# Kernel tuning notes

Measured on AMD Instinct MI355X. Metric: run time of the kernel, lower is better.

The kernel has to match this reference:

```python
import jax, jax.numpy as jnp
import numpy as np

N = 100_000   # nodes
C = 32        # classes
E = 3_200_000 # edges


def setup_inputs() -> dict:
    key = jax.random.key(0)
    k1, k2, k3, k4, k5 = jax.random.split(key, 5)
    edge_index = jax.random.randint(k1, (2, E), 0, N, dtype=jnp.int32)
    edge_weight = jax.random.uniform(k2, (E,), dtype=jnp.float32) + 0.1  # positive weights
    inputs = jax.random.normal(k3, (N, C), dtype=jnp.float32)
    labels = jax.random.randint(k4, (N,), 0, C)
    y = jax.nn.one_hot(labels, C, dtype=jnp.float32)  # torch.where(y[:, i]) implies one-hot labels
    sample_mask = jax.random.bernoulli(k5, 0.5, (N,))
    return {"edge_index": edge_index, "edge_weight": edge_weight,
            "inputs": inputs, "y": y, "sample_mask": sample_mask}


def _normalize_sparse(edge_index, edge_weight, n):
    # normalize_sparse_tensor: add self-loops (weight 1), then D^{-1/2} A D^{-1/2}
    loop = jnp.arange(n, dtype=edge_index.dtype)
    row = jnp.concatenate([edge_index[0], loop])
    col = jnp.concatenate([edge_index[1], loop])
    w = jnp.concatenate([edge_weight, jnp.ones((n,), edge_weight.dtype)])
    deg = jax.ops.segment_sum(w, row, num_segments=n)
    dinv = jnp.where(deg > 0, jax.lax.rsqrt(deg), 0.0)
    vals = dinv[row] * w * dinv[col]
    return row, col, vals


def reference(edge_index, edge_weight, inputs, y, sample_mask):
    n, c = inputs.shape
    row, col, vals = _normalize_sparse(edge_index, edge_weight, n)

    p = jax.nn.softmax(inputs, axis=1)
    m = sample_mask.astype(p.dtype)[:, None]
    p = p * (1.0 - m) + y * m          # replace predictions by labels on masked nodes
    ym = y * m                          # labels only on masked nodes

    # nodeH = raw_normed_adj @ p   (sparse spmm)  -> (n, c)
    nodeH = jax.ops.segment_sum(vals[:, None] * p[col], row, num_segments=n)

    # per-class mean of nodeH over nodes with label i (one-hot => sum/count)
    cnt = ym.sum(axis=0)                         # (c,)
    H = (ym.T @ nodeH) / cnt[:, None]            # (c, c); NaN rows if class empty

    # NaN fixups (identity when no NaNs present)
    Hn = jnp.isnan(H)
    H = jnp.where(Hn, H.T, H)
    Hn = jnp.isnan(H)
    H0 = jnp.where(Hn, jnp.zeros_like(H), H)
    miss = (1.0 - H0.sum(axis=1, keepdims=True)) / Hn.sum(axis=1, keepdims=True).astype(H.dtype)
    H = jnp.where(Hn, miss, H0)

    # makeDoubleStochasticH: iterate col-norm then row-norm; 'delta' = ||H||_1 (as in source)
    def cond(state):
        _, i, d = state
        return (d >= 1e-12) & (i < 3000)

    def body(state):
        Hc, i, _ = state
        Hc = Hc / Hc.sum(axis=0, keepdims=True)
        Hc = Hc / Hc.sum(axis=1, keepdims=True)
        return Hc, i + 1, jnp.abs(Hc).sum()

    H, _, _ = jax.lax.while_loop(cond, body, (H, jnp.int32(0), jnp.float32(1e30)))
    return H
```

## Files before the change

kernel.cpp:

```cpp
#include <hip/hip_runtime.h>
#include <hip/hip_fp16.h>


#define RS 32768
#define RSH 15
#define BDEG 64
#define W 200
#define NBKTMAX 512
#define BCAP 4608
#define LCAP 4096
#define NSC 512
#define NPR NBKTMAX
#define NTOT (1 + NPR)
#define NRED 16
#define RPER ((NTOT + NRED - 1) / NRED)
#define PPAD 204
#define BVW 3200

__global__ __launch_bounds__(1024) void
k_deg(const int* __restrict__ ei, const float* __restrict__ ew,
      __half* __restrict__ slab, const unsigned char* __restrict__ mask_bytes,
      int* __restrict__ flag, float* __restrict__ Hg, float* __restrict__ cnt,
      int* __restrict__ gCnt, int E_, int R) {
  __shared__ float h[RS];
  if (blockIdx.x == 0) {
    Hg[threadIdx.x] = 0.f;
    if (threadIdx.x < 32) cnt[threadIdx.x] = 0.f;
    if (threadIdx.x < NBKTMAX) gCnt[threadIdx.x] = 0;
    __shared__ int shi;
    if (threadIdx.x == 0) shi = 0;
    __syncthreads();
    int acc = mask_bytes[threadIdx.x * 4 + 1] | mask_bytes[threadIdx.x * 4 + 2]
            | mask_bytes[threadIdx.x * 4 + 3];
    if (acc) atomicOr(&shi, 1);
    __syncthreads();
    if (threadIdx.x == 0) *flag = (shi != 0) ? 1 : 0;
  }
  int r = blockIdx.x % R;
  int sl = blockIdx.x / R;
  for (int i = threadIdx.x; i < RS; i += 1024) h[i] = 0.f;
  __syncthreads();
  int lo = r << RSH;
  int Q = E_ >> 2;
  int q0 = (int)((long long)Q * sl / BDEG);
  int q1 = (int)((long long)Q * (sl + 1) / BDEG);
  const int4* ei4 = (const int4*)ei;
  const float4* ew4 = (const float4*)ew;
  int q = q0 + threadIdx.x;
  for (; q + 1024 < q1; q += 2048) {
    int4 ia = ei4[q], ib = ei4[q + 1024];
    float4 wa = ew4[q], wb = ew4[q + 1024];
    unsigned o0 = (unsigned)(ia.x - lo), o1 = (unsigned)(ia.y - lo);
    unsigned o2 = (unsigned)(ia.z - lo), o3 = (unsigned)(ia.w - lo);
    unsigned o4 = (unsigned)(ib.x - lo), o5 = (unsigned)(ib.y - lo);
    unsigned o6 = (unsigned)(ib.z - lo), o7 = (unsigned)(ib.w - lo);
    if (o0 < RS) atomicAdd(&h[o0], wa.x);
    if (o1 < RS) atomicAdd(&h[o1], wa.y);
    if (o2 < RS) atomicAdd(&h[o2], wa.z);
    if (o3 < RS) atomicAdd(&h[o3], wa.w);
    if (o4 < RS) atomicAdd(&h[o4], wb.x);
    if (o5 < RS) atomicAdd(&h[o5], wb.y);
    if (o6 < RS) atomicAdd(&h[o6], wb.z);
    if (o7 < RS) atomicAdd(&h[o7], wb.w);
  }
  for (; q < q1; q += 1024) {
    int4 idx = ei4[q];
    float4 w = ew4[q];
    unsigned o0 = (unsigned)(idx.x - lo), o1 = (unsigned)(idx.y - lo);
    unsigned o2 = (unsigned)(idx.z - lo), o3 = (unsigned)(idx.w - lo);
    if (o0 < RS) atomicAdd(&h[o0], w.x);
    if (o1 < RS) atomicAdd(&h[o1], w.y);
    if (o2 < RS) atomicAdd(&h[o2], w.z);
    if (o3 < RS) atomicAdd(&h[o3], w.w);
  }
  if (sl == BDEG - 1) {
    for (int e = (Q << 2) + threadIdx.x; e < E_; e += 1024) {
      unsigned off = (unsigned)(ei[e] - lo);
      if (off < RS) atomicAdd(&h[off], ew[e]);
    }
  }
  __syncthreads();
  __half* dst = slab + ((size_t)r * BDEG + sl) * RS;
  for (int i = threadIdx.x; i < RS; i += 1024) dst[i] = __float2half(h[i]);
}

__global__ void k_node(const float* __restrict__ x, const float* __restrict__ y,
                       const void* __restrict__ maskp, const int* __restrict__ flag,
                       const __half* __restrict__ slab, int2* __restrict__ ninfo,
                       __half* __restrict__ p16, float* __restrict__ Hg,
                       float* __restrict__ cnt, unsigned* __restrict__ bitvec, int Nn) {
  __shared__ float scnt[32], sdiag[32];
  if (threadIdx.x < 32) { scnt[threadIdx.x] = 0.f; sdiag[threadIdx.x] = 0.f; }
  __syncthreads();
  int n = blockIdx.x * blockDim.x + threadIdx.x;
  bool inb = (n < Nn);
  bool byteMask = (*flag != 0);
  bool msk = false;
  if (inb)
    msk = byteMask ? (((const unsigned char*)maskp)[n] != 0)
                   : (((const int*)maskp)[n] != 0);
  unsigned long long bm = __ballot(msk);
  if ((threadIdx.x & 63) == 0)
    ((unsigned long long*)bitvec)[n >> 6] = bm;
  if (inb) {
    const __half* sl = slab + ((size_t)(n >> RSH) * BDEG) * RS + (n & (RS - 1));
    float d = 0.f;
    #pragma unroll 8
    for (int bb = 0; bb < BDEG; ++bb) d += __half2float(sl[(size_t)bb * RS]);
    float dinv = rsqrtf(d + 1.0f);
    int a = -1;
    if (msk) {
      const float4* yi = (const float4*)(y + (size_t)n * 32);
      #pragma unroll
      for (int q = 0; q < 8; ++q) {
        float4 v = yi[q];
        if (v.x == 1.f) a = q * 4 + 0;
        if (v.y == 1.f) a = q * 4 + 1;
        if (v.z == 1.f) a = q * 4 + 2;
        if (v.w == 1.f) a = q * 4 + 3;
      }
      atomicAdd(&scnt[a], 1.f);
      atomicAdd(&sdiag[a], dinv * dinv);
    } else {
      const float4* xi = (const float4*)(x + (size_t)n * 32);
      float xs[32];
      #pragma unroll
      for (int q = 0; q < 8; ++q) {
        float4 v = xi[q];
        xs[q*4+0] = v.x; xs[q*4+1] = v.y; xs[q*4+2] = v.z; xs[q*4+3] = v.w;
      }
      float mx = -3.4e38f;
      #pragma unroll
      for (int i = 0; i < 32; ++i) mx = fmaxf(mx, xs[i]);
      float s = 0.f;
      #pragma unroll
      for (int i = 0; i < 32; ++i) { xs[i] = __expf(xs[i] - mx); s += xs[i]; }
      float inv = 1.f / s;
      union { short sh[32]; int4 v[4]; } u;
      #pragma unroll
      for (int i = 0; i < 32; ++i)
        u.sh[i] = __half_as_short(__float2half(xs[i] * inv));
      int4* po = (int4*)(p16 + (size_t)n * 32);
      #pragma unroll
      for (int q = 0; q < 4; ++q) po[q] = u.v[q];
    }
    int2 ni; ni.x = __float_as_int(dinv); ni.y = a;
    ninfo[n] = ni;
  }
  __syncthreads();
  if (threadIdx.x < 32) {
    if (scnt[threadIdx.x] != 0.f) atomicAdd(&cnt[threadIdx.x], scnt[threadIdx.x]);
    if (sdiag[threadIdx.x] != 0.f) atomicAdd(&Hg[threadIdx.x * 33], sdiag[threadIdx.x]);
  }
}

__global__ __launch_bounds__(1024) void
k_bucket(const int* __restrict__ ei, const float* __restrict__ ew,
         const int2* __restrict__ ninfo, const unsigned* __restrict__ bitvec,
         int2* __restrict__ gBucket, int* __restrict__ gCnt, int E_) {
  __shared__ int2 list[LCAP];
  __shared__ int lcnt;
  __shared__ int bcnt[NBKTMAX];
  __shared__ int gbase[NBKTMAX];
  __shared__ int bplace[NBKTMAX];
  __shared__ unsigned sbv[BVW];
  if (threadIdx.x == 0) lcnt = 0;
  if (threadIdx.x < NBKTMAX) { bcnt[threadIdx.x] = 0; bplace[threadIdx.x] = 0; }
  for (int i = threadIdx.x; i < BVW; i += 1024) sbv[i] = bitvec[i];
  __syncthreads();
  int E4 = E_ >> 2;
  int q0 = (int)((long long)E4 * blockIdx.x / NSC);
  int q1 = (int)((long long)E4 * (blockIdx.x + 1) / NSC);
  for (int q = q0 + threadIdx.x; q < q1; q += 1024) {
    int4 rr = ((const int4*)ei)[q];
    int4 cc = ((const int4*)(ei + E_))[q];
    float4 ww = ((const float4*)ew)[q];
    int rs[4] = {rr.x, rr.y, rr.z, rr.w};
    int cs[4] = {cc.x, cc.y, cc.z, cc.w};
    float wv[4] = {ww.x, ww.y, ww.z, ww.w};
    bool act[4];
    #pragma unroll
    for (int k = 0; k < 4; ++k)
      act[k] = (sbv[(unsigned)rs[k] >> 5] >> (rs[k] & 31)) & 1;
    int2 nr[4];
    #pragma unroll
    for (int k = 0; k < 4; ++k)
      if (act[k]) nr[k] = ninfo[rs[k]];
    #pragma unroll
    for (int k = 0; k < 4; ++k) {
      if (act[k]) {
        float val = __int_as_float(nr[k].x) * wv[k];
        int pos = atomicAdd(&lcnt, 1);
        if (pos < LCAP) list[pos] = make_int2((cs[k] << 5) | nr[k].y, __float_as_int(val));
      }
    }
  }
  if (blockIdx.x == NSC - 1) {
    for (int e = (E4 << 2) + threadIdx.x; e < E_; e += 1024) {
      int r = ei[e];
      if (!((sbv[(unsigned)r >> 5] >> (r & 31)) & 1)) continue;
      int2 nr = ninfo[r];
      int c = ei[E_ + e];
      float val = __int_as_float(nr.x) * ew[e];
      int pos = atomicAdd(&lcnt, 1);
      if (pos < LCAP) list[pos] = make_int2((c << 5) | nr.y, __float_as_int(val));
    }
  }
  __syncthreads();
  int nl = min(lcnt, LCAP);
  for (int i = threadIdx.x; i < nl; i += 1024)
    atomicAdd(&bcnt[(list[i].x >> 5) / W], 1);
  __syncthreads();
  if (threadIdx.x < NBKTMAX) {
    int n = bcnt[threadIdx.x];
    gbase[threadIdx.x] = (n > 0) ? atomicAdd(&gCnt[threadIdx.x], n) : 0;
  }
  __syncthreads();
  for (int i = threadIdx.x; i < nl; i += 1024) {
    int2 rec = list[i];
    int bkt = (rec.x >> 5) / W;
    int slot = atomicAdd(&bplace[bkt], 1);
    int dst = gbase[bkt] + slot;
    if (dst < BCAP) gBucket[(size_t)bkt * BCAP + dst] = rec;
  }
}

__global__ __launch_bounds__(1024) void
k_process(const int2* __restrict__ gBucket, const int* __restrict__ gCnt,
          const int2* __restrict__ ninfo, const __half* __restrict__ p16,
          float* __restrict__ procSlab, int Nn) {
  __shared__ float TlocT[32 * W];
  __shared__ __half plocT[32 * PPAD];
  __shared__ float H32[1024];
  __shared__ float ldin[W];
  __shared__ int   llab[W];
  int k = blockIdx.x;
  int c0 = k * W;
  int Wb = min(c0 + W, Nn) - c0;
  for (int i = threadIdx.x; i < 32 * W; i += 1024) TlocT[i] = 0.f;
  H32[threadIdx.x] = 0.f;
  if ((int)threadIdx.x < Wb) {
    int2 ni = ninfo[c0 + threadIdx.x];
    ldin[threadIdx.x] = __int_as_float(ni.x);
    llab[threadIdx.x] = ni.y;
  }
  __syncthreads();
  if (Wb > 0) {
    for (int i = threadIdx.x; i < Wb * 32; i += 1024) {
      int c = i >> 5, b = i & 31;
      plocT[b * PPAD + c] = p16[(size_t)(c0 + c) * 32 + b];
    }
    int n = min(gCnt[k], BCAP);
    const int2* bk = gBucket + (size_t)k * BCAP;
    for (int i = threadIdx.x; i < n; i += 1024) {
      int2 rec = bk[i];
      int cl = (rec.x >> 5) - c0;
      int a = rec.x & 31;
      float v = __int_as_float(rec.y) * ldin[cl];
      int b = llab[cl];
      if (b >= 0) atomicAdd(&H32[a * 32 + b], v);
      else        atomicAdd(&TlocT[a * W + cl], v);
    }
  }
  __syncthreads();
  int a = threadIdx.x >> 5;
  int b = threadIdx.x & 31;
  float acc0 = 0.f, acc1 = 0.f, acc2 = 0.f, acc3 = 0.f;
  int c = 0;
  for (; c + 3 < Wb; c += 4) {
    float4 tv = *(const float4*)&TlocT[a * W + c];
    short4 ps = *(const short4*)&plocT[b * PPAD + c];
    acc0 += tv.x * __half2float(__short_as_half(ps.x));
    acc1 += tv.y * __half2float(__short_as_half(ps.y));
    acc2 += tv.z * __half2float(__short_as_half(ps.z));
    acc3 += tv.w * __half2float(__short_as_half(ps.w));
  }
  for (; c < Wb; ++c)
    acc0 += TlocT[a * W + c] * __half2float(plocT[b * PPAD + c]);
  procSlab[(size_t)k * 1024 + threadIdx.x] =
      (acc0 + acc1) + (acc2 + acc3) + H32[threadIdx.x];
}

__global__ __launch_bounds__(1024) void
k_red(const float* __restrict__ allSlabs, float* __restrict__ red) {
  int k0 = blockIdx.x * RPER;
  int k1 = min(k0 + RPER, NTOT);
  float s = 0.f;
  for (int k = k0; k < k1; ++k) s += allSlabs[(size_t)k * 1024 + threadIdx.x];
  red[(size_t)blockIdx.x * 1024 + threadIdx.x] = s;
}

__global__ __launch_bounds__(1024) void
k_sinkhorn(const float* __restrict__ red, const float* __restrict__ cnt,
           float* __restrict__ out) {
  __shared__ float sHH[1024];
  int t = threadIdx.x;
  float s = 0.f;
  #pragma unroll
  for (int k = 0; k < NRED; ++k) s += red[(size_t)k * 1024 + t];
  sHH[t] = s;
  __syncthreads();
  int j = t;
  if (j >= 32) return;
  float cj = cnt[j];
  float Hcol[32], Hrow[32];
  #pragma unroll
  for (int i = 0; i < 32; ++i) Hcol[i] = sHH[i * 32 + j];
  #pragma unroll
  for (int i = 0; i < 32; ++i) Hcol[i] /= __shfl(cj, i);
  #pragma unroll
  for (int k = 0; k < 32; ++k) Hrow[k] = sHH[j * 32 + k] / cj;
  float u = 1.f, v = 1.f;
  for (int it = 0; it < 40; ++it) {
    float a0 = 0.f, a1 = 0.f, a2 = 0.f, a3 = 0.f;
    #pragma unroll
    for (int i = 0; i < 32; i += 4) {
      a0 += Hcol[i+0] * __shfl(u, i+0);
      a1 += Hcol[i+1] * __shfl(u, i+1);
      a2 += Hcol[i+2] * __shfl(u, i+2);
      a3 += Hcol[i+3] * __shfl(u, i+3);
    }
    v = 1.f / ((a0 + a1) + (a2 + a3));
    a0 = a1 = a2 = a3 = 0.f;
    #pragma unroll
    for (int k = 0; k < 32; k += 4) {
      a0 += Hrow[k+0] * __shfl(v, k+0);
      a1 += Hrow[k+1] * __shfl(v, k+1);
      a2 += Hrow[k+2] * __shfl(v, k+2);
      a3 += Hrow[k+3] * __shfl(v, k+3);
    }
    u = 1.f / ((a0 + a1) + (a2 + a3));
  }
  #pragma unroll
  for (int i = 0; i < 32; ++i) out[i * 32 + j] = __shfl(u, i) * Hcol[i] * v;
}

extern "C" void kernel_launch(void* const* d_in, const int* in_sizes, int n_in,
                              void* d_out, int out_size, void* d_ws, size_t ws_size,
                              hipStream_t stream) {
  const int*   ei   = (const int*)d_in[0];
  const float* ew   = (const float*)d_in[1];
  const float* x    = (const float*)d_in[2];
  const float* y    = (const float*)d_in[3];
  const void*  mask = d_in[4];
  float* out = (float*)d_out;
  int E_ = in_sizes[1];
  int Nn = in_sizes[2] / 32;
  int R = (Nn + RS - 1) >> RSH;

  char* ws = (char*)d_ws;
  size_t o = 0;
  float* cnt = (float*)(ws + o);    o += 128;
  int*   flag = (int*)(ws + o);     o += 128;
  int*   gCnt = (int*)(ws + o);     o += NBKTMAX * 4;
  float* allSlabs = (float*)(ws + o);
  float* Hg       = allSlabs;
  float* procSlab = allSlabs + 1024;
  o += (size_t)NTOT * 4096;
  float* red = (float*)(ws + o);    o += (size_t)NRED * 4096;
  int2*  gBucket = (int2*)(ws + o); o += (size_t)NBKTMAX * BCAP * 8;
  __half* slab = (__half*)(ws + o); o += (size_t)R * BDEG * RS * 2;
  int2*  ninfo = (int2*)(ws + o);   o += (size_t)Nn * 8;
  __half* p16 = (__half*)(ws + o);  o += (size_t)Nn * 64;
  unsigned* gbv = (unsigned*)(ws + o); o += (size_t)BVW * 4;

  int nb = (Nn + 255) / 256;
  k_deg<<<R * BDEG, 1024, 0, stream>>>(ei, ew, slab, (const unsigned char*)mask,
                                       flag, Hg, cnt, gCnt, E_, R);
  k_node<<<nb, 256, 0, stream>>>(x, y, mask, flag, slab, ninfo, p16, Hg, cnt, gbv, Nn);
  k_bucket<<<NSC, 1024, 0, stream>>>(ei, ew, ninfo, gbv, gBucket, gCnt, E_);
  k_process<<<NPR, 1024, 0, stream>>>(gBucket, gCnt, ninfo, p16, procSlab, Nn);
  k_red<<<NRED, 1024, 0, stream>>>(allSlabs, red);
  k_sinkhorn<<<1, 1024, 0, stream>>>(red, cnt, out);
}
```

Baseline: 219.1 us.

## Enlarge degree histogram ranges and coalesce bucket scatter via local sort

The degree kernel's per-block node range grows from 32768 to 40960 and the slice count changes, so that 3 ranges cover N with fewer idle bins and a different block count. The mask-flag scratch int now reuses the histogram shared array so the larger histogram still fits in LDS. In the bucket kernel, records are first locally sorted by bucket using a prefix scan into shared memory (reusing the bitvector region), then written out contiguously per bucket. This coalesces global writes at the cost of an extra shared-memory pass and scan barriers.

```diff
diff --git a/kernel.cpp b/kernel.cpp
--- a/kernel.cpp
+++ b/kernel.cpp
@@ -2,9 +2,8 @@
 #include <hip/hip_fp16.h>
 
 
-#define RS 32768
-#define RSH 15
-#define BDEG 64
+#define RS 40960
+#define BDEG 85
 #define W 200
 #define NBKTMAX 512
 #define BCAP 4608
@@ -16,6 +15,7 @@
 #define RPER ((NTOT + NRED - 1) / NRED)
 #define PPAD 204
 #define BVW 3200
+#define L2A (BVW / 2)
 
 __global__ __launch_bounds__(1024) void
 k_deg(const int* __restrict__ ei, const float* __restrict__ ew,
@@ -27,20 +27,20 @@
     Hg[threadIdx.x] = 0.f;
     if (threadIdx.x < 32) cnt[threadIdx.x] = 0.f;
     if (threadIdx.x < NBKTMAX) gCnt[threadIdx.x] = 0;
-    __shared__ int shi;
-    if (threadIdx.x == 0) shi = 0;
+    int* hi = (int*)h;
+    if (threadIdx.x == 0) hi[0] = 0;
     __syncthreads();
     int acc = mask_bytes[threadIdx.x * 4 + 1] | mask_bytes[threadIdx.x * 4 + 2]
             | mask_bytes[threadIdx.x * 4 + 3];
-    if (acc) atomicOr(&shi, 1);
+    if (acc) atomicOr(&hi[0], 1);
     __syncthreads();
-    if (threadIdx.x == 0) *flag = (shi != 0) ? 1 : 0;
+    if (threadIdx.x == 0) *flag = (hi[0] != 0) ? 1 : 0;
   }
   int r = blockIdx.x % R;
   int sl = blockIdx.x / R;
   for (int i = threadIdx.x; i < RS; i += 1024) h[i] = 0.f;
   __syncthreads();
-  int lo = r << RSH;
+  int lo = r * RS;
   int Q = E_ >> 2;
   int q0 = (int)((long long)Q * sl / BDEG);
   int q1 = (int)((long long)Q * (sl + 1) / BDEG);
@@ -103,9 +103,9 @@
   if ((threadIdx.x & 63) == 0)
     ((unsigned long long*)bitvec)[n >> 6] = bm;
   if (inb) {
-    const __half* sl = slab + ((size_t)(n >> RSH) * BDEG) * RS + (n & (RS - 1));
+    const __half* sl = slab + ((size_t)(n / RS) * BDEG) * RS + (n % RS);
     float d = 0.f;
-    #pragma unroll 8
+    #pragma unroll 5
     for (int bb = 0; bb < BDEG; ++bb) d += __half2float(sl[(size_t)bb * RS]);
     float dinv = rsqrtf(d + 1.0f);
     int a = -1;
@@ -163,10 +163,13 @@
   __shared__ int bcnt[NBKTMAX];
   __shared__ int gbase[NBKTMAX];
   __shared__ int bplace[NBKTMAX];
-  __shared__ unsigned sbv[BVW];
+  __shared__ int sbase[NBKTMAX];
+  union USH { unsigned sbv[BVW]; int2 l2[L2A]; };
+  __shared__ USH us;
+  __shared__ int2 l2b[LCAP - L2A];
   if (threadIdx.x == 0) lcnt = 0;
   if (threadIdx.x < NBKTMAX) { bcnt[threadIdx.x] = 0; bplace[threadIdx.x] = 0; }
-  for (int i = threadIdx.x; i < BVW; i += 1024) sbv[i] = bitvec[i];
+  for (int i = threadIdx.x; i < BVW; i += 1024) us.sbv[i] = bitvec[i];
   __syncthreads();
   int E4 = E_ >> 2;
   int q0 = (int)((long long)E4 * blockIdx.x / NSC);
@@ -181,7 +184,7 @@
     bool act[4];
     #pragma unroll
     for (int k = 0; k < 4; ++k)
-      act[k] = (sbv[(unsigned)rs[k] >> 5] >> (rs[k] & 31)) & 1;
+      act[k] = (us.sbv[(unsigned)rs[k] >> 5] >> (rs[k] & 31)) & 1;
     int2 nr[4];
     #pragma unroll
     for (int k = 0; k < 4; ++k)
@@ -198,7 +201,7 @@
   if (blockIdx.x == NSC - 1) {
     for (int e = (E4 << 2) + threadIdx.x; e < E_; e += 1024) {
       int r = ei[e];
-      if (!((sbv[(unsigned)r >> 5] >> (r & 31)) & 1)) continue;
+      if (!((us.sbv[(unsigned)r >> 5] >> (r & 31)) & 1)) continue;
       int2 nr = ninfo[r];
       int c = ei[E_ + e];
       float val = __int_as_float(nr.x) * ew[e];
@@ -211,6 +214,15 @@
   for (int i = threadIdx.x; i < nl; i += 1024)
     atomicAdd(&bcnt[(list[i].x >> 5) / W], 1);
   __syncthreads();
+  if (threadIdx.x < NBKTMAX) sbase[threadIdx.x] = bcnt[threadIdx.x];
+  __syncthreads();
+  for (int off = 1; off < NBKTMAX; off <<= 1) {
+    int v = 0;
+    if (threadIdx.x < NBKTMAX && threadIdx.x >= off) v = sbase[threadIdx.x - off];
+    __syncthreads();
+    if (threadIdx.x < NBKTMAX && threadIdx.x >= off) sbase[threadIdx.x] += v;
+    __syncthreads();
+  }
   if (threadIdx.x < NBKTMAX) {
     int n = bcnt[threadIdx.x];
     gbase[threadIdx.x] = (n > 0) ? atomicAdd(&gCnt[threadIdx.x], n) : 0;
@@ -219,8 +231,14 @@
   for (int i = threadIdx.x; i < nl; i += 1024) {
     int2 rec = list[i];
     int bkt = (rec.x >> 5) / W;
-    int slot = atomicAdd(&bplace[bkt], 1);
-    int dst = gbase[bkt] + slot;
+    int d = sbase[bkt] - bcnt[bkt] + atomicAdd(&bplace[bkt], 1);
+    if (d < L2A) us.l2[d] = rec; else l2b[d - L2A] = rec;
+  }
+  __syncthreads();
+  for (int j = threadIdx.x; j < nl; j += 1024) {
+    int2 rec = (j < L2A) ? us.l2[j] : l2b[j - L2A];
+    int bkt = (rec.x >> 5) / W;
+    int dst = gbase[bkt] + (j - (sbase[bkt] - bcnt[bkt]));
     if (dst < BCAP) gBucket[(size_t)bkt * BCAP + dst] = rec;
   }
 }
@@ -346,7 +364,7 @@
   float* out = (float*)d_out;
   int E_ = in_sizes[1];
   int Nn = in_sizes[2] / 32;
-  int R = (Nn + RS - 1) >> RSH;
+  int R = (Nn + RS - 1) / RS;
 
   char* ws = (char*)d_ws;
   size_t o = 0;
```

New measurement: 218.8 us. Within noise of the previous version (-0.1%).
